# Performance work log

Hardware: AMD Instinct MI355X
Metric: run time of the kernel (lower is better)

## Reference

```python
import jax, jax.numpy as jnp
import numpy as np

Q, A, R, S, K = 256, 28, 512, 256, 2  # n_quantize, n_aux, n_resch, n_skipch, kernel_size
DEPTH, REPEAT = 10, 3
L = DEPTH * REPEAT  # 30 layers
T = 8192


def setup_inputs() -> dict:
    key = jax.random.key(0)
    ks = jax.random.split(key, 24)
    w = lambda k, shape: jax.random.normal(k, shape, dtype=jnp.float32) * 0.05
    return {
        "x": jax.random.randint(ks[0], (1, T), 0, Q, dtype=jnp.int32),
        "h": jax.random.normal(ks[1], (1, A, T), dtype=jnp.float32),
        "Wc": w(ks[2], (R, Q, K)), "bc": w(ks[3], (R,)),
        "Wds": w(ks[4], (L, R, R, K)), "bds": w(ks[5], (L, R)),
        "Wdt": w(ks[6], (L, R, R, K)), "bdt": w(ks[7], (L, R)),
        "Was": w(ks[8], (L, R, A, 1)), "bas": w(ks[9], (L, R)),
        "Wat": w(ks[10], (L, R, A, 1)), "bat": w(ks[11], (L, R)),
        "Wsk": w(ks[12], (L, S, R, 1)), "bsk": w(ks[13], (L, S)),
        "Wr": w(ks[14], (L, R, R, 1)), "br": w(ks[15], (L, R)),
        "Wp1": w(ks[16], (S, S, 1)), "bp1": w(ks[17], (S,)),
        "Wp2": w(ks[18], (Q, S, 1)), "bp2": w(ks[19], (Q,)),
    }


def _cconv(z, w, b, d):
    # causal dilated conv: z [1,C,T], w [O,C,K] -> [1,O,T]
    pad = (w.shape[2] - 1) * d
    y = jax.lax.conv_general_dilated(
        z, w, window_strides=(1,), padding=[(pad, 0)], rhs_dilation=(d,),
        dimension_numbers=("NCH", "OIH", "NCH"))
    return y + b[None, :, None]


def reference(x, h, Wc, bc, Wds, bds, Wdt, bdt, Was, bas, Wat, bat,
              Wsk, bsk, Wr, br, Wp1, bp1, Wp2, bp2):
    dilations = [2 ** i for i in range(DEPTH)] * REPEAT
    oh = jax.nn.one_hot(x, Q, dtype=Wc.dtype).transpose(0, 2, 1)  # [1,Q,T]
    out = _cconv(oh, Wc, bc, 1)  # [1,R,T]
    skip_sum = jnp.zeros((1, S, oh.shape[2]), dtype=Wc.dtype)
    for l, d in enumerate(dilations):
        s = _cconv(out, Wds[l], bds[l], d) + _cconv(h, Was[l], bas[l], 1)
        t = _cconv(out, Wdt[l], bdt[l], d) + _cconv(h, Wat[l], bat[l], 1)
        g = jax.nn.sigmoid(s) * jnp.tanh(t)  # gated activation
        skip_sum = skip_sum + _cconv(g, Wsk[l], bsk[l], 1)
        out = _cconv(g, Wr[l], br[l], 1) + out  # residual
    o = jax.nn.relu(skip_sum)
    o = jax.nn.relu(_cconv(o, Wp1, bp1, 1))
    o = _cconv(o, Wp2, bp2, 1)  # [1,Q,T]
    return o[0].T  # [T,Q], matches squeeze(0).transpose(0,1)
```

## Files before the change

kernel.cpp:

```cpp
#include <hip/hip_runtime.h>
#include <hip/hip_bf16.h>
#include <math.h>
#include <stdint.h>

#define T_LEN 8192
#define RCH   512
#define SCH   256
#define QCH   256
#define ACH   28
#define NLAYER 30
#define KGATE 1088
#define KSR   512
#define KPOST 256

typedef _Float16 f16x8 __attribute__((ext_vector_type(8)));
typedef float    f32x4 __attribute__((ext_vector_type(4)));

#define SB0() __builtin_amdgcn_sched_barrier(0)

static __device__ __forceinline__ unsigned short f2h(float v) {
    _Float16 h = (_Float16)v;
    return *reinterpret_cast<unsigned short*>(&h);
}

static __device__ __forceinline__ float fsig(float x) {
    return __builtin_amdgcn_rcpf(1.f + __expf(-x));
}

#define G2L(SRC, DST) __builtin_amdgcn_global_load_lds(                        \
    (__attribute__((address_space(1))) void*)(const void*)(SRC),              \
    (__attribute__((address_space(3))) void*)(void*)(DST), 16, 0, 0)

__global__ void pack_gated_v(const float* __restrict__ Wds,
                             const float* __restrict__ Wdt,
                             unsigned short* __restrict__ dst) {
    int l = blockIdx.y;
    int c = blockIdx.x * 256 + threadIdx.x;
    int mlow = c & 15;
    int kg   = (c >> 4) & 63;
    int mhi  = c >> 10;
    int m  = mhi * 16 + mlow;
    int k0 = kg * 8;
    int br = m & 1, ch = m >> 1;
    const float* Wd = (br ? Wdt : Wds) + (size_t)l * RCH * RCH * 2
                    + ((size_t)ch * 512 + k0) * 2;
    unsigned short o0[8], o1[8];
    #pragma unroll
    for (int q = 0; q < 4; ++q) {
        float4 v = *(const float4*)(Wd + q * 4);
        o0[q * 2 + 0] = f2h(v.x); o1[q * 2 + 0] = f2h(v.y);
        o0[q * 2 + 1] = f2h(v.z); o1[q * 2 + 1] = f2h(v.w);
    }
    int mt   = m >> 4;
    int lane = ((k0 & 31) >> 3) * 16 + mlow;
    int kt0  = k0 >> 5;
    size_t base = (size_t)l * 1024 * KGATE;
    *(uint4*)&dst[base + (size_t)(mt * 34 + kt0)      * 512 + lane * 8] = *(uint4*)o0;
    *(uint4*)&dst[base + (size_t)(mt * 34 + kt0 + 16) * 512 + lane * 8] = *(uint4*)o1;
}

__global__ void pack_gatea_v(const float* __restrict__ Was,
                             const float* __restrict__ Wat,
                             unsigned short* __restrict__ dst) {
    int l = blockIdx.y;
    int c = blockIdx.x * 256 + threadIdx.x;
    int mlow = c & 15;
    int kg   = (c >> 4) & 7;
    int mhi  = c >> 7;
    int m  = mhi * 16 + mlow;
    int a0 = kg * 8;
    int br = m & 1, ch = m >> 1;
    const float* Wa = (br ? Wat : Was) + (size_t)l * RCH * ACH + (size_t)ch * ACH;
    unsigned short o[8];
    #pragma unroll
    for (int i = 0; i < 8; ++i)
        o[i] = (a0 + i < ACH) ? f2h(Wa[a0 + i]) : (unsigned short)0;
    int mt   = m >> 4;
    int lane = ((a0 & 31) >> 3) * 16 + mlow;
    *(uint4*)&dst[(size_t)l * 1024 * KGATE
                  + (size_t)(mt * 34 + 32 + (a0 >> 5)) * 512 + lane * 8] = *(uint4*)o;
}

__global__ void pack_sr_v(const float* __restrict__ Wsk,
                          const float* __restrict__ Wr,
                          unsigned short* __restrict__ dst) {
    int l = blockIdx.y;
    int c = blockIdx.x * 256 + threadIdx.x;
    int tile = c >> 6, lane = c & 63;
    int mt = tile >> 4, kt = tile & 15;
    int m  = mt * 16 + (lane & 15);
    int k0 = kt * 32 + (lane >> 4) * 8;
    const float* row = (m < SCH) ? (Wsk + (size_t)l * SCH * RCH + (size_t)m * 512)
                                 : (Wr  + (size_t)l * RCH * RCH + (size_t)(m - SCH) * 512);
    float4 v0 = *(const float4*)(row + k0);
    float4 v1 = *(const float4*)(row + k0 + 4);
    unsigned short o[8] = { f2h(v0.x), f2h(v0.y), f2h(v0.z), f2h(v0.w),
                            f2h(v1.x), f2h(v1.y), f2h(v1.z), f2h(v1.w) };
    *(uint4*)&dst[(size_t)l * 768 * KSR + (size_t)tile * 512 + lane * 8] = *(uint4*)o;
}

__global__ void pack_post_v(const float* __restrict__ W,
                            unsigned short* __restrict__ dst) {
    int c = blockIdx.x * 256 + threadIdx.x;
    int tile = c >> 6, lane = c & 63;
    int mt = tile >> 3, kt = tile & 7;
    int m  = mt * 16 + (lane & 15);
    int k0 = kt * 32 + (lane >> 4) * 8;
    float4 v0 = *(const float4*)(W + (size_t)m * 256 + k0);
    float4 v1 = *(const float4*)(W + (size_t)m * 256 + k0 + 4);
    unsigned short o[8] = { f2h(v0.x), f2h(v0.y), f2h(v0.z), f2h(v0.w),
                            f2h(v1.x), f2h(v1.y), f2h(v1.z), f2h(v1.w) };
    *(uint4*)&dst[(size_t)tile * 512 + lane * 8] = *(uint4*)o;
}

__global__ void transpose_wc(const float* __restrict__ Wc,
                             float* __restrict__ WcT) {
    int idx = blockIdx.x * 256 + threadIdx.x;
    int r = idx >> 9;
    int qt = idx & 511;
    int q = qt >> 1, tap = qt & 1;
    WcT[(size_t)q * 1024 + tap * 512 + r] = Wc[(size_t)r * 512 + qt];
}

__global__ void embed_v(const int* __restrict__ x,
                        const float* __restrict__ WcT,
                        const float* __restrict__ bc,
                        float* __restrict__ out_tm,
                        unsigned short* __restrict__ outhf) {
    int idx = blockIdx.x * 256 + threadIdx.x;
    int t = idx >> 6, rc = (idx & 63) * 8;
    int x1 = x[t];
    const float* w1 = WcT + (size_t)x1 * 1024 + 512 + rc;
    float4 a = *(const float4*)w1;
    float4 b = *(const float4*)(w1 + 4);
    float4 c0 = *(const float4*)(bc + rc);
    float4 c1 = *(const float4*)(bc + rc + 4);
    a.x += c0.x; a.y += c0.y; a.z += c0.z; a.w += c0.w;
    b.x += c1.x; b.y += c1.y; b.z += c1.z; b.w += c1.w;
    if (t > 0) {
        const float* w0 = WcT + (size_t)x[t - 1] * 1024 + rc;
        float4 d0 = *(const float4*)w0;
        float4 d1 = *(const float4*)(w0 + 4);
        a.x += d0.x; a.y += d0.y; a.z += d0.z; a.w += d0.w;
        b.x += d1.x; b.y += d1.y; b.z += d1.z; b.w += d1.w;
    }
    size_t o = (size_t)t * 512 + rc;
    *(float4*)&out_tm[o] = a;
    *(float4*)&out_tm[o + 4] = b;
    unsigned short p[8] = { f2h(a.x), f2h(a.y), f2h(a.z), f2h(a.w),
                            f2h(b.x), f2h(b.y), f2h(b.z), f2h(b.w) };
    *(uint4*)&outhf[o + 512 * 512] = *(uint4*)p;
}

__global__ void packh_kernel(const float* __restrict__ h,
                             unsigned short* __restrict__ h_tm) {
    int idx = blockIdx.x * 256 + threadIdx.x;
    int t = idx >> 6, a = idx & 63;
    h_tm[idx] = f2h(a < ACH ? h[(size_t)a * T_LEN + t] : 0.f);
}

__global__ void reluconv_v(const float* __restrict__ skip,
                           unsigned short* __restrict__ dst) {
    int idx = (blockIdx.x * 256 + threadIdx.x) * 8;
    float4 v0 = *(const float4*)(skip + idx);
    float4 v1 = *(const float4*)(skip + idx + 4);
    unsigned short o[8] = { f2h(fmaxf(v0.x, 0.f)), f2h(fmaxf(v0.y, 0.f)),
                            f2h(fmaxf(v0.z, 0.f)), f2h(fmaxf(v0.w, 0.f)),
                            f2h(fmaxf(v1.x, 0.f)), f2h(fmaxf(v1.y, 0.f)),
                            f2h(fmaxf(v1.z, 0.f)), f2h(fmaxf(v1.w, 0.f)) };
    *(uint4*)&dst[idx] = *(uint4*)o;
}

template<int MODE, int KT64, int MB>
__global__ __launch_bounds__(256) void mfma_gemm(
    const unsigned short* __restrict__ Apk,
    const unsigned short* __restrict__ B0,
    const unsigned short* __restrict__ B2,
    const float* __restrict__ bias0, const float* __restrict__ bias1,
    const float* __restrict__ bias2, const float* __restrict__ bias3,
    float* __restrict__ O0, float* __restrict__ O1,
    unsigned short* __restrict__ OB, int dil)
{
    constexpr int KT32 = KT64 * 2;
    constexpr int NWG = MB * 64;
    constexpr int CPX = NWG / 8;

    __shared__ unsigned short Bsm[2][128 * 64];

    const int tid  = threadIdx.x;
    const int lane = tid & 63, wave = tid >> 6;

    const int bid = blockIdx.x;
    const int swz = (bid & 7) * CPX + (bid >> 3);
    const int mb  = swz % MB;
    const int tb  = swz / MB;
    const int m0  = mb * 128;
    const int t0  = tb * 128;

    const int kc   = ((lane & 7) ^ (lane >> 3)) * 8;
    const int rsub = lane >> 3;

    const size_t mt0 = (size_t)(mb * 8) + wave * 2;

    f32x4 acc[2][8];
    #pragma unroll
    for (int a = 0; a < 2; ++a)
        #pragma unroll
        for (int b = 0; b < 8; ++b) acc[a][b] = (f32x4){0.f, 0.f, 0.f, 0.f};

    f16x8 afrA[2][2], afrB[2][2], bfr[8][2];

    auto stage_tile = [&](int kt, int buf) {
        const int kb = kt * 64;
        #pragma unroll
        for (int j = 0; j < 4; ++j) {
            const int row = wave * 32 + j * 8 + rsub;
            const int tg  = t0 + row;
            const unsigned short* src;
            if constexpr (MODE == 0) {
                if (kb < 512)
                    src = B0 + (size_t)(512 + tg - dil) * 512 + kb + kc;
                else if (kb < 1024)
                    src = B0 + (size_t)(512 + tg) * 512 + (kb - 512) + kc;
                else
                    src = B2 + (size_t)tg * 64 + kc;
            } else if constexpr (MODE == 1) {
                src = B0 + (size_t)tg * 512 + kb + kc;
            } else {
                src = B0 + (size_t)tg * 256 + kb + kc;
            }
            G2L(src, &Bsm[buf][(wave * 4 + j) * 512]);
        }
    };

    auto load_afr = [&](int kt, f16x8 (&dst)[2][2]) {
        #pragma unroll
        for (int mi = 0; mi < 2; ++mi)
            #pragma unroll
            for (int ks = 0; ks < 2; ++ks)
                dst[mi][ks] = *(const f16x8*)(Apk +
                    ((mt0 + mi) * KT32 + (size_t)(kt * 2 + ks)) * 512 + lane * 8);
    };

    auto load_bfr = [&](int buf) {
        #pragma unroll
        for (int ni = 0; ni < 8; ++ni)
            #pragma unroll
            for (int ks = 0; ks < 2; ++ks) {
                const int trow = ni * 16 + (lane & 15);
                const int kch  = ks * 4 + (lane >> 4);
                const int sch  = kch ^ (lane & 7);
                bfr[ni][ks] = *(const f16x8*)&Bsm[buf][trow * 64 + sch * 8];
            }
    };

    auto do_mfma = [&](f16x8 (&A)[2][2]) {
        __builtin_amdgcn_s_setprio(1);
        #pragma unroll
        for (int mi = 0; mi < 2; ++mi)
            #pragma unroll
            for (int ni = 0; ni < 8; ++ni) {
                acc[mi][ni] = __builtin_amdgcn_mfma_f32_16x16x32_f16(
                    A[mi][0], bfr[ni][0], acc[mi][ni], 0, 0, 0);
                acc[mi][ni] = __builtin_amdgcn_mfma_f32_16x16x32_f16(
                    A[mi][1], bfr[ni][1], acc[mi][ni], 0, 0, 0);
            }
        __builtin_amdgcn_s_setprio(0);
    };

    stage_tile(0, 0);
    SB0();
    load_afr(0, afrA);
    SB0();
    asm volatile("s_waitcnt vmcnt(4)" ::: "memory");
    SB0();
    __builtin_amdgcn_s_barrier();

    #pragma unroll
    for (int kt = 0; kt < KT64; ++kt) {
        const int cur = kt & 1;
        if (kt + 1 < KT64) {
            stage_tile(kt + 1, cur ^ 1);
            SB0();
            if (cur) load_afr(kt + 1, afrA);
            else     load_afr(kt + 1, afrB);
            SB0();
        }
        load_bfr(cur);
        if (cur) do_mfma(afrB);
        else     do_mfma(afrA);
        if (kt + 1 < KT64) {
            SB0();
            asm volatile("s_waitcnt vmcnt(4) lgkmcnt(0)" ::: "memory");
            SB0();
            __builtin_amdgcn_s_barrier();
        }
    }

    const int rb0 = (lane >> 4) * 4;
    #pragma unroll
    for (int mi = 0; mi < 2; ++mi) {
        #pragma unroll
        for (int ni = 0; ni < 8; ++ni) {
            int m = m0 + wave * 32 + mi * 16 + rb0;
            int t = t0 + ni * 16 + (lane & 15);
            f32x4 v = acc[mi][ni];
            if constexpr (MODE == 0) {
                int c0 = m >> 1;
                float s0 = v.x + bias0[c0]     + bias2[c0];
                float tv0 = v.y + bias1[c0]     + bias3[c0];
                float s1 = v.z + bias0[c0 + 1] + bias2[c0 + 1];
                float tv1 = v.w + bias1[c0 + 1] + bias3[c0 + 1];
                float g0 = fsig(s0) * (2.f * fsig(2.f * tv0) - 1.f);
                float g1 = fsig(s1) * (2.f * fsig(2.f * tv1) - 1.f);
                unsigned int p = (unsigned int)f2h(g0) | ((unsigned int)f2h(g1) << 16);
                *(unsigned int*)&OB[(size_t)t * 512 + c0] = p;
            } else if constexpr (MODE == 1) {
                if (m < SCH) {
                    float4* p = (float4*)&O0[(size_t)t * 256 + m];
                    float4 o = *p;
                    o.x += v.x + bias0[m + 0];
                    o.y += v.y + bias0[m + 1];
                    o.z += v.z + bias0[m + 2];
                    o.w += v.w + bias0[m + 3];
                    *p = o;
                } else {
                    int c = m - SCH;
                    float4* p = (float4*)&O1[(size_t)t * 512 + c];
                    float4 o = *p;
                    o.x += v.x + bias1[c + 0];
                    o.y += v.y + bias1[c + 1];
                    o.z += v.z + bias1[c + 2];
                    o.w += v.w + bias1[c + 3];
                    *p = o;
                    uint2 pk;
                    pk.x = (unsigned int)f2h(o.x) | ((unsigned int)f2h(o.y) << 16);
                    pk.y = (unsigned int)f2h(o.z) | ((unsigned int)f2h(o.w) << 16);
                    *(uint2*)&OB[(size_t)(512 + t) * 512 + c] = pk;
                }
            } else if constexpr (MODE == 2) {
                float o0 = fmaxf(v.x + bias0[m + 0], 0.f);
                float o1 = fmaxf(v.y + bias0[m + 1], 0.f);
                float o2 = fmaxf(v.z + bias0[m + 2], 0.f);
                float o3 = fmaxf(v.w + bias0[m + 3], 0.f);
                uint2 pk;
                pk.x = (unsigned int)f2h(o0) | ((unsigned int)f2h(o1) << 16);
                pk.y = (unsigned int)f2h(o2) | ((unsigned int)f2h(o3) << 16);
                *(uint2*)&OB[(size_t)t * 256 + m] = pk;
            } else {
                float4 o;
                o.x = v.x + bias0[m + 0];
                o.y = v.y + bias0[m + 1];
                o.z = v.z + bias0[m + 2];
                o.w = v.w + bias0[m + 3];
                *(float4*)&O0[(size_t)t * 256 + m] = o;
            }
        }
    }
}

extern "C" void kernel_launch(void* const* d_in, const int* in_sizes, int n_in,
                              void* d_out, int out_size, void* d_ws, size_t ws_size,
                              hipStream_t stream) {
    const int*   x   = (const int*)  d_in[0];
    const float* h   = (const float*)d_in[1];
    const float* Wc  = (const float*)d_in[2];
    const float* bc  = (const float*)d_in[3];
    const float* Wds = (const float*)d_in[4];
    const float* bds = (const float*)d_in[5];
    const float* Wdt = (const float*)d_in[6];
    const float* bdt = (const float*)d_in[7];
    const float* Was = (const float*)d_in[8];
    const float* bas = (const float*)d_in[9];
    const float* Wat = (const float*)d_in[10];
    const float* bat = (const float*)d_in[11];
    const float* Wsk = (const float*)d_in[12];
    const float* bsk = (const float*)d_in[13];
    const float* Wr  = (const float*)d_in[14];
    const float* br  = (const float*)d_in[15];
    const float* Wp1 = (const float*)d_in[16];
    const float* bp1 = (const float*)d_in[17];
    const float* Wp2 = (const float*)d_in[18];
    const float* bp2 = (const float*)d_in[19];
    float* dout = (float*)d_out;

    const size_t WG_EL  = (size_t)1024 * KGATE;
    const size_t WSR_EL = (size_t)768 * KSR;
    char* w = (char*)d_ws;
    float*          out_tm = (float*)w;               w += (size_t)T_LEN * 512 * 4;
    unsigned short* outhf  = (unsigned short*)w;      w += (size_t)(T_LEN + 512) * 512 * 2;
    unsigned short* g_tm   = (unsigned short*)w;      w += (size_t)T_LEN * 512 * 2;
    unsigned short* h_tm   = (unsigned short*)w;      w += (size_t)T_LEN * 64 * 2;
    unsigned short* skiphf = (unsigned short*)w;      w += (size_t)T_LEN * 256 * 2;
    unsigned short* o1hf   = (unsigned short*)w;      w += (size_t)T_LEN * 256 * 2;
    unsigned short* Wp1_pk = (unsigned short*)w;      w += (size_t)256 * 256 * 2;
    unsigned short* Wp2_pk = (unsigned short*)w;      w += (size_t)256 * 256 * 2;
    float*          WcT    = (float*)w;               w += (size_t)QCH * 2 * RCH * 4;
    unsigned short* Wg_pk  = (unsigned short*)w;
    size_t used_base = (size_t)((char*)Wg_pk - (char*)d_ws);
    size_t need_bulk = used_base + (WG_EL + WSR_EL) * NLAYER * 2;
    const bool bulk = ws_size >= need_bulk;
    unsigned short* Wsr_pk = Wg_pk + (bulk ? WG_EL * NLAYER : WG_EL);
    float* skip = dout;

    hipMemsetAsync(skip, 0, (size_t)T_LEN * 256 * 4, stream);
    hipMemsetAsync(outhf, 0, (size_t)512 * 512 * 2, stream);

    transpose_wc<<<1024, 256, 0, stream>>>(Wc, WcT);
    embed_v<<<(T_LEN * 64) / 256, 256, 0, stream>>>(x, WcT, bc, out_tm, outhf);
    packh_kernel<<<(T_LEN * 64) / 256, 256, 0, stream>>>(h, h_tm);
    pack_post_v<<<32, 256, 0, stream>>>(Wp1, Wp1_pk);
    pack_post_v<<<32, 256, 0, stream>>>(Wp2, Wp2_pk);

    if (bulk) {
        pack_gated_v<<<dim3(256, NLAYER), 256, 0, stream>>>(Wds, Wdt, Wg_pk);
        pack_gatea_v<<<dim3(32, NLAYER), 256, 0, stream>>>(Was, Wat, Wg_pk);
        pack_sr_v<<<dim3(192, NLAYER), 256, 0, stream>>>(Wsk, Wr, Wsr_pk);
    }

    for (int l = 0; l < NLAYER; ++l) {
        int dil = 1 << (l % 10);
        const unsigned short* wg;
        const unsigned short* wsr;
        if (bulk) {
            wg  = Wg_pk  + (size_t)l * WG_EL;
            wsr = Wsr_pk + (size_t)l * WSR_EL;
        } else {
            pack_gated_v<<<dim3(256, 1), 256, 0, stream>>>(
                Wds + (size_t)l * RCH * RCH * 2, Wdt + (size_t)l * RCH * RCH * 2, Wg_pk);
            pack_gatea_v<<<dim3(32, 1), 256, 0, stream>>>(
                Was + (size_t)l * RCH * ACH, Wat + (size_t)l * RCH * ACH, Wg_pk);
            pack_sr_v<<<dim3(192, 1), 256, 0, stream>>>(
                Wsk + (size_t)l * SCH * RCH, Wr + (size_t)l * RCH * RCH, Wsr_pk);
            wg = Wg_pk; wsr = Wsr_pk;
        }
        mfma_gemm<0, KGATE / 64, 8><<<512, 256, 0, stream>>>(
            wg, outhf, h_tm,
            bds + (size_t)l * RCH, bdt + (size_t)l * RCH,
            bas + (size_t)l * RCH, bat + (size_t)l * RCH,
            nullptr, nullptr, g_tm, dil);
        mfma_gemm<1, KSR / 64, 6><<<384, 256, 0, stream>>>(
            wsr, g_tm, nullptr,
            bsk + (size_t)l * SCH, br + (size_t)l * RCH, nullptr, nullptr,
            skip, out_tm, outhf, 0);
    }

    reluconv_v<<<(T_LEN * 256 / 8) / 256, 256, 0, stream>>>(skip, skiphf);
    mfma_gemm<2, KPOST / 64, 2><<<128, 256, 0, stream>>>(
        Wp1_pk, skiphf, nullptr, bp1, nullptr, nullptr, nullptr,
        nullptr, nullptr, o1hf, 0);
    mfma_gemm<3, KPOST / 64, 2><<<128, 256, 0, stream>>>(
        Wp2_pk, o1hf, nullptr, bp2, nullptr, nullptr, nullptr,
        dout, nullptr, nullptr, 0);
}
```

Baseline: 1.427 ms.

## Stage gated weight packing through LDS and interleave B-fragment loads with MFMA

Rewrites the gated-weight packing kernel to read the fp32 weights with coalesced float4 loads into an LDS tile, then emit the MFMA-packed fp16 layout with contiguous 16-byte stores. In the GEMM, B fragments are now loaded per column block right before their MFMAs instead of all up front, which cuts live registers. A launch-bounds hint of three blocks per CU is added to raise occupancy. The trade-off is that each MFMA group now waits on LDS reads more directly, and the register cap may force spills.

After: 1.462 ms. 2.4% more time.

```diff
diff --git a/kernel.cpp b/kernel.cpp
--- a/kernel.cpp
+++ b/kernel.cpp
@@ -12,6 +12,7 @@
 #define KGATE 1088
 #define KSR   512
 #define KPOST 256
+#define PSTR  1032
 
 typedef _Float16 f16x8 __attribute__((ext_vector_type(8)));
 typedef float    f32x4 __attribute__((ext_vector_type(4)));
@@ -31,32 +32,46 @@
     (__attribute__((address_space(1))) void*)(const void*)(SRC),              \
     (__attribute__((address_space(3))) void*)(void*)(DST), 16, 0, 0)
 
-__global__ void pack_gated_v(const float* __restrict__ Wds,
-                             const float* __restrict__ Wdt,
-                             unsigned short* __restrict__ dst) {
-    int l = blockIdx.y;
-    int c = blockIdx.x * 256 + threadIdx.x;
-    int mlow = c & 15;
-    int kg   = (c >> 4) & 63;
-    int mhi  = c >> 10;
-    int m  = mhi * 16 + mlow;
-    int k0 = kg * 8;
-    int br = m & 1, ch = m >> 1;
-    const float* Wd = (br ? Wdt : Wds) + (size_t)l * RCH * RCH * 2
-                    + ((size_t)ch * 512 + k0) * 2;
-    unsigned short o0[8], o1[8];
-    #pragma unroll
-    for (int q = 0; q < 4; ++q) {
-        float4 v = *(const float4*)(Wd + q * 4);
-        o0[q * 2 + 0] = f2h(v.x); o1[q * 2 + 0] = f2h(v.y);
-        o0[q * 2 + 1] = f2h(v.z); o1[q * 2 + 1] = f2h(v.w);
-    }
-    int mt   = m >> 4;
-    int lane = ((k0 & 31) >> 3) * 16 + mlow;
-    int kt0  = k0 >> 5;
-    size_t base = (size_t)l * 1024 * KGATE;
-    *(uint4*)&dst[base + (size_t)(mt * 34 + kt0)      * 512 + lane * 8] = *(uint4*)o0;
-    *(uint4*)&dst[base + (size_t)(mt * 34 + kt0 + 16) * 512 + lane * 8] = *(uint4*)o1;
+__global__ void pack_gated_lds(const float* __restrict__ Wds,
+                               const float* __restrict__ Wdt,
+                               unsigned short* __restrict__ dst) {
+    __shared__ unsigned short L[16 * PSTR];
+    const int l  = blockIdx.y;
+    const int mt = blockIdx.x;
+    const int t  = threadIdx.x;
+
+    const float* S0 = Wds + (size_t)l * RCH * RCH * 2 + (size_t)mt * 8 * 1024;
+    const float* S1 = Wdt + (size_t)l * RCH * RCH * 2 + (size_t)mt * 8 * 1024;
+
+    #pragma unroll
+    for (int br = 0; br < 2; ++br) {
+        const float* S = br ? S1 : S0;
+        #pragma unroll
+        for (int r = 0; r < 8; ++r) {
+            int fidx = (r * 256 + t) * 4;
+            float4 v = *(const float4*)(S + fidx);
+            int ch_off = fidx >> 10;
+            int k = (fidx & 1023) >> 1;
+            int g = ch_off * 2 + br;
+            unsigned int p0 = (unsigned int)f2h(v.x) | ((unsigned int)f2h(v.z) << 16);
+            unsigned int p1 = (unsigned int)f2h(v.y) | ((unsigned int)f2h(v.w) << 16);
+            *(unsigned int*)&L[g * PSTR + k]       = p0;
+            *(unsigned int*)&L[g * PSTR + 512 + k] = p1;
+        }
+    }
+    __syncthreads();
+
+    size_t base = (size_t)l * 1024 * KGATE + (size_t)mt * 34 * 512;
+    #pragma unroll
+    for (int w = 0; w < 8; ++w) {
+        int idx  = w * 256 + t;
+        int kt   = idx >> 6;
+        int lane = idx & 63;
+        int g    = lane & 15;
+        int koff = kt * 32 + (lane >> 4) * 8;
+        uint4 v = *(uint4*)&L[g * PSTR + koff];
+        *(uint4*)&dst[base + (size_t)kt * 512 + lane * 8] = v;
+    }
 }
 
 __global__ void pack_gatea_v(const float* __restrict__ Was,
@@ -172,7 +187,7 @@
 }
 
 template<int MODE, int KT64, int MB>
-__global__ __launch_bounds__(256) void mfma_gemm(
+__global__ __launch_bounds__(256, 3) void mfma_gemm(
     const unsigned short* __restrict__ Apk,
     const unsigned short* __restrict__ B0,
     const unsigned short* __restrict__ B2,
@@ -208,7 +223,7 @@
         #pragma unroll
         for (int b = 0; b < 8; ++b) acc[a][b] = (f32x4){0.f, 0.f, 0.f, 0.f};
 
-    f16x8 afrA[2][2], afrB[2][2], bfr[8][2];
+    f16x8 afrA[2][2], afrB[2][2];
 
     auto stage_tile = [&](int kt, int buf) {
         const int kb = kt * 64;
@@ -242,29 +257,22 @@
                     ((mt0 + mi) * KT32 + (size_t)(kt * 2 + ks)) * 512 + lane * 8);
     };
 
-    auto load_bfr = [&](int buf) {
-        #pragma unroll
-        for (int ni = 0; ni < 8; ++ni)
+    auto compute = [&](int buf, f16x8 (&A)[2][2]) {
+        __builtin_amdgcn_s_setprio(1);
+        #pragma unroll
+        for (int ni = 0; ni < 8; ++ni) {
+            const int trow = ni * 16 + (lane & 15);
+            const int kch0 = lane >> 4;
+            f16x8 b0 = *(const f16x8*)&Bsm[buf][trow * 64 + ((kch0    ) ^ (lane & 7)) * 8];
+            f16x8 b1 = *(const f16x8*)&Bsm[buf][trow * 64 + ((kch0 + 4) ^ (lane & 7)) * 8];
             #pragma unroll
-            for (int ks = 0; ks < 2; ++ks) {
-                const int trow = ni * 16 + (lane & 15);
-                const int kch  = ks * 4 + (lane >> 4);
-                const int sch  = kch ^ (lane & 7);
-                bfr[ni][ks] = *(const f16x8*)&Bsm[buf][trow * 64 + sch * 8];
+            for (int mi = 0; mi < 2; ++mi) {
+                acc[mi][ni] = __builtin_amdgcn_mfma_f32_16x16x32_f16(
+                    A[mi][0], b0, acc[mi][ni], 0, 0, 0);
+                acc[mi][ni] = __builtin_amdgcn_mfma_f32_16x16x32_f16(
+                    A[mi][1], b1, acc[mi][ni], 0, 0, 0);
             }
-    };
-
-    auto do_mfma = [&](f16x8 (&A)[2][2]) {
-        __builtin_amdgcn_s_setprio(1);
-        #pragma unroll
-        for (int mi = 0; mi < 2; ++mi)
-            #pragma unroll
-            for (int ni = 0; ni < 8; ++ni) {
-                acc[mi][ni] = __builtin_amdgcn_mfma_f32_16x16x32_f16(
-                    A[mi][0], bfr[ni][0], acc[mi][ni], 0, 0, 0);
-                acc[mi][ni] = __builtin_amdgcn_mfma_f32_16x16x32_f16(
-                    A[mi][1], bfr[ni][1], acc[mi][ni], 0, 0, 0);
-            }
+        }
         __builtin_amdgcn_s_setprio(0);
     };
 
@@ -286,9 +294,8 @@
             else     load_afr(kt + 1, afrB);
             SB0();
         }
-        load_bfr(cur);
-        if (cur) do_mfma(afrB);
-        else     do_mfma(afrA);
+        if (cur) compute(cur, afrB);
+        else     compute(cur, afrA);
         if (kt + 1 < KT64) {
             SB0();
             asm volatile("s_waitcnt vmcnt(4) lgkmcnt(0)" ::: "memory");
@@ -413,7 +420,7 @@
     pack_post_v<<<32, 256, 0, stream>>>(Wp2, Wp2_pk);
 
     if (bulk) {
-        pack_gated_v<<<dim3(256, NLAYER), 256, 0, stream>>>(Wds, Wdt, Wg_pk);
+        pack_gated_lds<<<dim3(64, NLAYER), 256, 0, stream>>>(Wds, Wdt, Wg_pk);
         pack_gatea_v<<<dim3(32, NLAYER), 256, 0, stream>>>(Was, Wat, Wg_pk);
         pack_sr_v<<<dim3(192, NLAYER), 256, 0, stream>>>(Wsk, Wr, Wsr_pk);
     }
@@ -426,7 +433,7 @@
             wg  = Wg_pk  + (size_t)l * WG_EL;
             wsr = Wsr_pk + (size_t)l * WSR_EL;
         } else {
-            pack_gated_v<<<dim3(256, 1), 256, 0, stream>>>(
+            pack_gated_lds<<<dim3(64, 1), 256, 0, stream>>>(
                 Wds + (size_t)l * RCH * RCH * 2, Wdt + (size_t)l * RCH * RCH * 2, Wg_pk);
             pack_gatea_v<<<dim3(32, 1), 256, 0, stream>>>(
                 Was + (size_t)l * RCH * ACH, Wat + (size_t)l * RCH * ACH, Wg_pk);
```
